# Performance work log

Measured on AMD Instinct MI355X. Metric: run time of the kernel, lower is better.

Reference implementation:

```python
import jax, jax.numpy as jnp
import numpy as np

MARGIN = 0.1


def setup_inputs() -> dict:
    key = jax.random.key(0)
    k1, k2 = jax.random.split(key)
    n, d, n_classes = 8192, 128, 512
    x = jax.random.normal(k1, (n, d), dtype=jnp.float32)
    # L2-normalize embeddings (cosine similarity regime, consistent with 0.6 threshold)
    x = x / jnp.linalg.norm(x, axis=1, keepdims=True)
    targets = jax.random.randint(k2, (n,), 0, n_classes, dtype=jnp.int64)
    return {"inputs": x, "targets": targets}


def reference(inputs, targets):
    n = inputs.shape[0]
    sim = inputs @ inputs.T                                   # [n, n]
    same = targets[:, None] == targets[None, :]               # label equality
    eye = jnp.eye(n, dtype=bool)
    pos_mask = same & ~eye                                    # positives, diag removed
    neg_mask = ~same                                          # negatives (diag excluded: same label)

    neg_inf = jnp.float32(-jnp.inf)
    max_neg = jnp.max(jnp.where(neg_mask, sim, neg_inf), axis=1)   # neg_pair_[-1]
    max_pos = jnp.max(jnp.where(pos_mask, sim, neg_inf), axis=1)   # pos_pair_[-1]

    # select positives with sim < max_neg + margin ; loss = sum(1 - sim)
    pos_sel = pos_mask & (sim < (max_neg + MARGIN)[:, None])
    pos_loss = jnp.sum(jnp.where(pos_sel, 1.0 - sim, 0.0), axis=1)

    # select negatives with sim > max(0.6, max_pos) - margin ; loss = sum(sim)
    thr = jnp.maximum(jnp.float32(0.6), max_pos) - MARGIN
    neg_sel = neg_mask & (sim > thr[:, None])
    neg_loss = jnp.sum(jnp.where(neg_sel, sim, 0.0), axis=1)

    has_pos = jnp.any(pos_mask, axis=1)
    loss = jnp.sum(jnp.where(has_pos, pos_loss + neg_loss, 0.0)) / n

    # diagnostics from the last row (as in the torch code's trailing pos_pair_/neg_pair_)
    lp = pos_mask[-1]
    ln = neg_mask[-1]
    mean_pos_sim = jnp.sum(jnp.where(lp, sim[-1], 0.0)) / jnp.maximum(jnp.sum(lp), 1)
    mean_neg_sim = jnp.sum(jnp.where(ln, sim[-1], 0.0)) / jnp.maximum(jnp.sum(ln), 1)
    zero = jnp.float32(0.0)
    return (loss, zero, zero, zero, mean_pos_sim, mean_neg_sim)
```

## Files before the change

### kernel.cpp

```cpp
#include <hip/hip_runtime.h>

typedef __attribute__((ext_vector_type(8))) short short8;
typedef __attribute__((ext_vector_type(4))) float f32x4;

#define D 128
#define MARGIN 0.1f
#define MAXC 64
#define FCAP 256

__device__ __forceinline__ unsigned short f32_to_bf16(float f) {
  unsigned int u = __float_as_uint(f);
  u += 0x7fffu + ((u >> 16) & 1u);
  return (unsigned short)(u >> 16);
}
__device__ __forceinline__ unsigned fkey(float f) {
  unsigned b = __float_as_uint(f);
  return b ^ (((unsigned)((int)b >> 31)) | 0x80000000u);
}
__device__ __forceinline__ float fdec(unsigned k) {
  unsigned b = k ^ ((k & 0x80000000u) ? 0x80000000u : 0xFFFFFFFFu);
  return __uint_as_float(b);
}

__global__ void k_prep(const float* __restrict__ x, unsigned short* __restrict__ xb,
                       unsigned* __restrict__ mn_u, int* __restrict__ cls_cnt, int n) {
  int gid = blockIdx.x * 256 + threadIdx.x;
  int i = gid * 4;
  float4 v = *reinterpret_cast<const float4*>(x + i);
  ushort4 o;
  o.x = f32_to_bf16(v.x);
  o.y = f32_to_bf16(v.y);
  o.z = f32_to_bf16(v.z);
  o.w = f32_to_bf16(v.w);
  *reinterpret_cast<ushort4*>(xb + i) = o;
  if (gid < n) mn_u[gid] = 0u;
  if (gid < 512) cls_cnt[gid] = 0;
}

#define MF(A, B, C) __builtin_amdgcn_mfma_f32_16x16x32_bf16(A, B, C, 0, 0, 0)

__launch_bounds__(256)
__global__ void k_main(const unsigned short* __restrict__ xb, const int* __restrict__ tg,
                       unsigned* __restrict__ mn_u,
                       int* __restrict__ cls_cnt, int* __restrict__ cls_idx, int n) {
  const int nrb = n >> 8;
  const int ngemm = nrb * 16;
  const int tid = threadIdx.x;
  if ((int)blockIdx.x >= ngemm) {
    int i = ((int)blockIdx.x - ngemm) * 256 + tid;
    if (i < n) {
      int c = tg[i];
      int s = atomicAdd(&cls_cnt[c], 1);
      if (s < MAXC) cls_idx[c * MAXC + s] = i;
    }
    return;
  }

  __shared__ uint4 ldsbuf[4096];
  char* lds = (char*)ldsbuf;
  const int lane = tid & 63;
  const int wid = tid >> 6;
  const int rb = blockIdx.x % nrb;
  const int colpart = blockIdx.x / nrb;
  const int r0 = rb << 8;
  const int cg = lane & 15;
  const int agrp = lane >> 4;

  short8 a[4][4];
#pragma unroll
  for (int rt = 0; rt < 4; ++rt)
#pragma unroll
    for (int kk = 0; kk < 4; ++kk)
      a[rt][kk] = *reinterpret_cast<const short8*>(
          xb + (size_t)(r0 + wid * 64 + rt * 16 + cg) * D + kk * 32 + agrp * 8);

  float mn[4][4];
#pragma unroll
  for (int rt = 0; rt < 4; ++rt)
#pragma unroll
    for (int reg = 0; reg < 4; ++reg) mn[rt][reg] = -INFINITY;

  const int skey = (((tid >> 4) & 7) << 4);
  const char* gbase = (const char*)xb + (size_t)colpart * 512 * 256;

  {
    uint4 v[8];
#pragma unroll
    for (int q = 0; q < 8; ++q)
      v[q] = *reinterpret_cast<const uint4*>(gbase + q * 4096 + tid * 16);
#pragma unroll
    for (int q = 0; q < 8; ++q)
      *reinterpret_cast<uint4*>(lds + ((q * 4096 + tid * 16) ^ skey)) = v[q];
  }
  __syncthreads();

  const int rowbase = r0 + wid * 64 + agrp * 4;

  int rofs[4];
#pragma unroll
  for (int kk = 0; kk < 4; ++kk)
    rofs[kk] = (cg * 256 + agrp * 16 + kk * 64) ^ ((cg & 7) << 4);

#pragma unroll
  for (int s = 0; s < 4; ++s) {
    uint4 g[8];
    if (s + 1 < 4) {
      const char* gs = gbase + (size_t)(s + 1) * 32768;
#pragma unroll
      for (int q = 0; q < 8; ++q)
        g[q] = *reinterpret_cast<const uint4*>(gs + q * 4096 + tid * 16);
    }
    const char* bb = lds + (s & 1) * 32768;
    const int cs = colpart * 4 + s;
    const bool hasdiag = ((cs >> 1) == rb);
    if (!hasdiag) {
#pragma unroll
      for (int j = 0; j < 8; ++j) {
        const char* tb = bb + j * 4096;
        short8 B[4];
#pragma unroll
        for (int kk = 0; kk < 4; ++kk)
          B[kk] = *reinterpret_cast<const short8*>(tb + rofs[kk]);
#pragma unroll
        for (int rt = 0; rt < 4; ++rt) {
          f32x4 acc = {0.f, 0.f, 0.f, 0.f};
          acc = MF(a[rt][0], B[0], acc);
          acc = MF(a[rt][1], B[1], acc);
          acc = MF(a[rt][2], B[2], acc);
          acc = MF(a[rt][3], B[3], acc);
#pragma unroll
          for (int reg = 0; reg < 4; ++reg)
            mn[rt][reg] = fmaxf(mn[rt][reg], acc[reg]);
        }
      }
    } else {
      const int ebase = rowbase - ((cs << 7) + cg);
#pragma unroll
      for (int j = 0; j < 8; ++j) {
        const char* tb = bb + j * 4096;
        short8 B[4];
#pragma unroll
        for (int kk = 0; kk < 4; ++kk)
          B[kk] = *reinterpret_cast<const short8*>(tb + rofs[kk]);
        const int e = ebase - j * 16;
#pragma unroll
        for (int rt = 0; rt < 4; ++rt) {
          f32x4 acc = {0.f, 0.f, 0.f, 0.f};
          acc = MF(a[rt][0], B[0], acc);
          acc = MF(a[rt][1], B[1], acc);
          acc = MF(a[rt][2], B[2], acc);
          acc = MF(a[rt][3], B[3], acc);
#pragma unroll
          for (int reg = 0; reg < 4; ++reg) {
            float v = (e + rt * 16 + reg == 0) ? -INFINITY : acc[reg];
            mn[rt][reg] = fmaxf(mn[rt][reg], v);
          }
        }
      }
    }
    if (s + 1 < 4) {
      char* wb = lds + ((s + 1) & 1) * 32768;
#pragma unroll
      for (int q = 0; q < 8; ++q)
        *reinterpret_cast<uint4*>(wb + ((q * 4096 + tid * 16) ^ skey)) = g[q];
      __syncthreads();
    }
  }

#pragma unroll
  for (int m = 1; m < 16; m <<= 1)
#pragma unroll
    for (int rt = 0; rt < 4; ++rt)
#pragma unroll
      for (int reg = 0; reg < 4; ++reg)
        mn[rt][reg] = fmaxf(mn[rt][reg], __shfl_xor(mn[rt][reg], m, 16));

  if (cg == 0) {
#pragma unroll
    for (int rt = 0; rt < 4; ++rt)
#pragma unroll
      for (int reg = 0; reg < 4; ++reg)
        atomicMax(&mn_u[rowbase + rt * 16 + reg], fkey(mn[rt][reg]));
  }
}

__global__ void k_posdiag(const float* __restrict__ x, const int* __restrict__ tg,
                          const unsigned* __restrict__ mn_u,
                          const int* __restrict__ cls_cnt, const int* __restrict__ cls_idx,
                          float* __restrict__ thn, float* __restrict__ pos_part,
                          float* __restrict__ dpart, int n) {
  __shared__ float red2[4][4];
  int lane = threadIdx.x & 63, wid = threadIdx.x >> 6;
  int nposb = n / 4;
  if ((int)blockIdx.x < nposb) {
    int r = blockIdx.x * 4 + wid;
    int tr = tg[r];
    float2 xr = *reinterpret_cast<const float2*>(x + (size_t)r * D + lane * 2);
    float thp = fdec(mn_u[r]) + MARGIN;
    int cnt = cls_cnt[tr];
    int m = cnt < MAXC ? cnt : MAXC;
    float mpos = -INFINITY, pl = 0.f;
    for (int k = 0; k < m; ++k) {
      int j = cls_idx[tr * MAXC + k];
      if (j == r) continue;
      float2 xj = *reinterpret_cast<const float2*>(x + (size_t)j * D + lane * 2);
      float d = xr.x * xj.x + xr.y * xj.y;
#pragma unroll
      for (int mm = 1; mm < 64; mm <<= 1) d += __shfl_xor(d, mm, 64);
      mpos = fmaxf(mpos, d);
      if (d < thp) pl += 1.0f - d;
    }
    bool has_pos = cnt > 1;
    if (lane == 0) {
      thn[r] = has_pos ? (fmaxf(0.6f, mpos) - MARGIN) : INFINITY;
      pos_part[r] = has_pos ? pl : 0.f;
    }
  } else {
    int col = (blockIdx.x - nposb) * 256 + threadIdx.x;
    int R = n - 1;
    int tR = tg[R];
    const float4* xr = reinterpret_cast<const float4*>(x + (size_t)R * D);
    const float4* xc = reinterpret_cast<const float4*>(x + (size_t)col * D);
    float dot = 0.f;
#pragma unroll
    for (int k = 0; k < D / 4; ++k) {
      float4 va = xr[k], vb = xc[k];
      dot += va.x * vb.x + va.y * vb.y + va.z * vb.z + va.w * vb.w;
    }
    int t = tg[col];
    bool same = (t == tR);
    bool isR = (col == R);
    float v[4];
    v[0] = (same && !isR) ? dot : 0.f;
    v[1] = (same && !isR) ? 1.f : 0.f;
    v[2] = (!same) ? dot : 0.f;
    v[3] = (!same) ? 1.f : 0.f;
#pragma unroll
    for (int m = 1; m < 64; m <<= 1)
#pragma unroll
      for (int j = 0; j < 4; ++j) v[j] += __shfl_xor(v[j], m, 64);
    if (lane == 0) {
#pragma unroll
      for (int j = 0; j < 4; ++j) red2[wid][j] = v[j];
    }
    __syncthreads();
    if (threadIdx.x == 0) {
#pragma unroll
      for (int j = 0; j < 4; ++j)
        dpart[(blockIdx.x - nposb) * 4 + j] =
            red2[0][j] + red2[1][j] + red2[2][j] + red2[3][j];
    }
  }
}

__global__ void k_final(const float* __restrict__ x, const int* __restrict__ tg,
                        const float* __restrict__ pos_part,
                        const unsigned* __restrict__ mn_u, const float* __restrict__ thn,
                        const float* __restrict__ dpart, int ndiag,
                        float* __restrict__ out, int n) {
  __shared__ int flags[FCAP];
  __shared__ int nflag;
  if (threadIdx.x == 0) nflag = 0;
  __syncthreads();
  float s = 0.f;
  for (int i = threadIdx.x; i < n; i += 256) {
    s += pos_part[i];
    if (fdec(mn_u[i]) > thn[i] - 0.02f) {
      int k = atomicAdd(&nflag, 1);
      if (k < FCAP) flags[k] = i;
    }
  }
  __syncthreads();
  int m = nflag < FCAP ? nflag : FCAP;
  for (int f = 0; f < m; ++f) {
    int r = flags[f];
    int trr = tg[r];
    float tv = thn[r];
    const float4* xr = reinterpret_cast<const float4*>(x + (size_t)r * D);
    for (int c = threadIdx.x; c < n; c += 256) {
      if (tg[c] == trr) continue;
      const float4* xc = reinterpret_cast<const float4*>(x + (size_t)c * D);
      float dot = 0.f;
#pragma unroll
      for (int k = 0; k < D / 4; ++k) {
        float4 va = xr[k], vb = xc[k];
        dot += va.x * vb.x + va.y * vb.y + va.z * vb.z + va.w * vb.w;
      }
      if (dot > tv) s += dot;
    }
  }
  int lane = threadIdx.x & 63, wid = threadIdx.x >> 6;
#pragma unroll
  for (int mm = 1; mm < 64; mm <<= 1) s += __shfl_xor(s, mm, 64);
  __shared__ float red[4];
  if (lane == 0) red[wid] = s;
  __syncthreads();
  if (threadIdx.x == 0) {
    float loss = red[0] + red[1] + red[2] + red[3];
    float ps = 0.f, pc = 0.f, ns = 0.f, nc = 0.f;
    for (int b = 0; b < ndiag; ++b) {
      ps += dpart[b * 4 + 0];
      pc += dpart[b * 4 + 1];
      ns += dpart[b * 4 + 2];
      nc += dpart[b * 4 + 3];
    }
    out[0] = loss / (float)n;
    out[1] = 0.f;
    out[2] = 0.f;
    out[3] = 0.f;
    out[4] = ps / fmaxf(pc, 1.f);
    out[5] = ns / fmaxf(nc, 1.f);
  }
}

extern "C" void kernel_launch(void* const* d_in, const int* in_sizes, int n_in,
                              void* d_out, int out_size, void* d_ws, size_t ws_size,
                              hipStream_t stream) {
  const float* x = (const float*)d_in[0];
  const int* tg = (const int*)d_in[1];
  float* out = (float*)d_out;
  int n = in_sizes[1];

  char* ws = (char*)d_ws;
  unsigned short* xb = (unsigned short*)ws;
  size_t off = (size_t)n * D * 2;
  unsigned* mn_u = (unsigned*)(ws + off); off += (size_t)n * 4;
  float* thn = (float*)(ws + off); off += (size_t)n * 4;
  int* cls_cnt = (int*)(ws + off); off += 512 * 4;
  int* cls_idx = (int*)(ws + off); off += 512 * MAXC * 4;
  float* pos_part = (float*)(ws + off); off += (size_t)n * 4;
  float* dpart = (float*)(ws + off);

  int total = n * D;
  int nrb = n >> 8;
  int ngemm = nrb * 16;
  k_prep<<<total / 1024, 256, 0, stream>>>(x, xb, mn_u, cls_cnt, n);
  k_main<<<ngemm + nrb, 256, 0, stream>>>(xb, tg, mn_u, cls_cnt, cls_idx, n);
  int nposb = n / 4, ndiag = n / 256;
  k_posdiag<<<nposb + ndiag, 256, 0, stream>>>(x, tg, mn_u, cls_cnt, cls_idx,
                                               thn, pos_part, dpart, n);
  k_final<<<1, 256, 0, stream>>>(x, tg, pos_part, mn_u, thn, dpart, ndiag, out, n);
}
```

Before: 72.72 us.

## Fuse all stages into one cooperative persistent kernel with grid syncs

Replaces the four separate kernel launches (prep, GEMM-max, positive/diagonal, final) with a single cooperative kernel of 256 blocks that separates the stages with grid-wide syncs. Each block now covers twice as many column stripes in the GEMM stage and two rounds of rows in the positive stage, which uses 16-lane groups instead of full waves. This removes launch gaps and inter-kernel overhead. In exchange, grid.sync costs are added, the GEMM runs with only 256 blocks at lower occupancy, and the sizes are hardcoded for n=8192.

```diff
diff --git a/kernel.cpp b/kernel.cpp
--- a/kernel.cpp
+++ b/kernel.cpp
@@ -1,4 +1,7 @@
 #include <hip/hip_runtime.h>
+#include <hip/hip_cooperative_groups.h>
+
+namespace cg = cooperative_groups;
 
 typedef __attribute__((ext_vector_type(8))) short short8;
 typedef __attribute__((ext_vector_type(4))) float f32x4;
@@ -22,294 +25,297 @@
   return __uint_as_float(b);
 }
 
-__global__ void k_prep(const float* __restrict__ x, unsigned short* __restrict__ xb,
-                       unsigned* __restrict__ mn_u, int* __restrict__ cls_cnt, int n) {
-  int gid = blockIdx.x * 256 + threadIdx.x;
-  int i = gid * 4;
-  float4 v = *reinterpret_cast<const float4*>(x + i);
-  ushort4 o;
-  o.x = f32_to_bf16(v.x);
-  o.y = f32_to_bf16(v.y);
-  o.z = f32_to_bf16(v.z);
-  o.w = f32_to_bf16(v.w);
-  *reinterpret_cast<ushort4*>(xb + i) = o;
-  if (gid < n) mn_u[gid] = 0u;
-  if (gid < 512) cls_cnt[gid] = 0;
-}
-
 #define MF(A, B, C) __builtin_amdgcn_mfma_f32_16x16x32_bf16(A, B, C, 0, 0, 0)
 
 __launch_bounds__(256)
-__global__ void k_main(const unsigned short* __restrict__ xb, const int* __restrict__ tg,
-                       unsigned* __restrict__ mn_u,
-                       int* __restrict__ cls_cnt, int* __restrict__ cls_idx, int n) {
-  const int nrb = n >> 8;
-  const int ngemm = nrb * 16;
+__global__ void k_all(const float* __restrict__ x, const int* __restrict__ tg,
+                      unsigned short* __restrict__ xb, unsigned* __restrict__ mn_u,
+                      float* __restrict__ thn, int* __restrict__ cls_cnt,
+                      int* __restrict__ cls_idx, float* __restrict__ pos_part,
+                      float* __restrict__ dpart, float* __restrict__ out, int n) {
+  cg::grid_group grid = cg::this_grid();
+  __shared__ uint4 ldsbuf[4096];
+  __shared__ float red2[4][4];
+  __shared__ float redf[4];
+  __shared__ int flags[FCAP];
+  __shared__ int nflag;
+
   const int tid = threadIdx.x;
-  if ((int)blockIdx.x >= ngemm) {
-    int i = ((int)blockIdx.x - ngemm) * 256 + tid;
-    if (i < n) {
+  const int bid = blockIdx.x;
+  const int gid = bid * 256 + tid;
+  const int lane = tid & 63;
+  const int wid = tid >> 6;
+
+  {
+    int i0 = gid * 16;
+#pragma unroll
+    for (int q = 0; q < 4; ++q) {
+      float4 v = *reinterpret_cast<const float4*>(x + i0 + q * 4);
+      ushort4 o;
+      o.x = f32_to_bf16(v.x);
+      o.y = f32_to_bf16(v.y);
+      o.z = f32_to_bf16(v.z);
+      o.w = f32_to_bf16(v.w);
+      *reinterpret_cast<ushort4*>(xb + i0 + q * 4) = o;
+    }
+    if (gid < n) mn_u[gid] = 0u;
+    if (gid < 512) cls_cnt[gid] = 0;
+  }
+  grid.sync();
+
+  {
+    if (tid < 32) {
+      int i = bid * 32 + tid;
       int c = tg[i];
       int s = atomicAdd(&cls_cnt[c], 1);
       if (s < MAXC) cls_idx[c * MAXC + s] = i;
     }
-    return;
-  }
-
-  __shared__ uint4 ldsbuf[4096];
-  char* lds = (char*)ldsbuf;
-  const int lane = tid & 63;
-  const int wid = tid >> 6;
-  const int rb = blockIdx.x % nrb;
-  const int colpart = blockIdx.x / nrb;
-  const int r0 = rb << 8;
-  const int cg = lane & 15;
-  const int agrp = lane >> 4;
-
-  short8 a[4][4];
-#pragma unroll
-  for (int rt = 0; rt < 4; ++rt)
+
+    const int nrb = n >> 8;
+    const int rb = bid % nrb;
+    const int cp0 = bid / nrb;
+    const int r0 = rb << 8;
+    const int cgl = lane & 15;
+    const int agrp = lane >> 4;
+    char* lds = (char*)ldsbuf;
+
+    short8 a[4][4];
+#pragma unroll
+    for (int rt = 0; rt < 4; ++rt)
+#pragma unroll
+      for (int kk = 0; kk < 4; ++kk)
+        a[rt][kk] = *reinterpret_cast<const short8*>(
+            xb + (size_t)(r0 + wid * 64 + rt * 16 + cgl) * D + kk * 32 + agrp * 8);
+
+    float mn[4][4];
+#pragma unroll
+    for (int rt = 0; rt < 4; ++rt)
+#pragma unroll
+      for (int reg = 0; reg < 4; ++reg) mn[rt][reg] = -INFINITY;
+
+    const int skey = (((tid >> 4) & 7) << 4);
+    const int rowbase = r0 + wid * 64 + agrp * 4;
+
+#define CS_OF(s) ((((s) < 4) ? cp0 : cp0 + 8) * 4 + ((s) & 3))
+
+    {
+      const char* gs = (const char*)xb + (size_t)CS_OF(0) * 32768;
+      uint4 v[8];
+#pragma unroll
+      for (int q = 0; q < 8; ++q)
+        v[q] = *reinterpret_cast<const uint4*>(gs + q * 4096 + tid * 16);
+#pragma unroll
+      for (int q = 0; q < 8; ++q)
+        *reinterpret_cast<uint4*>(lds + ((q * 4096 + tid * 16) ^ skey)) = v[q];
+    }
+    __syncthreads();
+
+    int rofs[4];
 #pragma unroll
     for (int kk = 0; kk < 4; ++kk)
-      a[rt][kk] = *reinterpret_cast<const short8*>(
-          xb + (size_t)(r0 + wid * 64 + rt * 16 + cg) * D + kk * 32 + agrp * 8);
-
-  float mn[4][4];
-#pragma unroll
-  for (int rt = 0; rt < 4; ++rt)
-#pragma unroll
-    for (int reg = 0; reg < 4; ++reg) mn[rt][reg] = -INFINITY;
-
-  const int skey = (((tid >> 4) & 7) << 4);
-  const char* gbase = (const char*)xb + (size_t)colpart * 512 * 256;
-
-  {
-    uint4 v[8];
-#pragma unroll
-    for (int q = 0; q < 8; ++q)
-      v[q] = *reinterpret_cast<const uint4*>(gbase + q * 4096 + tid * 16);
-#pragma unroll
-    for (int q = 0; q < 8; ++q)
-      *reinterpret_cast<uint4*>(lds + ((q * 4096 + tid * 16) ^ skey)) = v[q];
-  }
-  __syncthreads();
-
-  const int rowbase = r0 + wid * 64 + agrp * 4;
-
-  int rofs[4];
-#pragma unroll
-  for (int kk = 0; kk < 4; ++kk)
-    rofs[kk] = (cg * 256 + agrp * 16 + kk * 64) ^ ((cg & 7) << 4);
-
-#pragma unroll
-  for (int s = 0; s < 4; ++s) {
-    uint4 g[8];
-    if (s + 1 < 4) {
-      const char* gs = gbase + (size_t)(s + 1) * 32768;
-#pragma unroll
-      for (int q = 0; q < 8; ++q)
-        g[q] = *reinterpret_cast<const uint4*>(gs + q * 4096 + tid * 16);
-    }
-    const char* bb = lds + (s & 1) * 32768;
-    const int cs = colpart * 4 + s;
-    const bool hasdiag = ((cs >> 1) == rb);
-    if (!hasdiag) {
-#pragma unroll
-      for (int j = 0; j < 8; ++j) {
-        const char* tb = bb + j * 4096;
-        short8 B[4];
-#pragma unroll
-        for (int kk = 0; kk < 4; ++kk)
-          B[kk] = *reinterpret_cast<const short8*>(tb + rofs[kk]);
-#pragma unroll
-        for (int rt = 0; rt < 4; ++rt) {
-          f32x4 acc = {0.f, 0.f, 0.f, 0.f};
-          acc = MF(a[rt][0], B[0], acc);
-          acc = MF(a[rt][1], B[1], acc);
-          acc = MF(a[rt][2], B[2], acc);
-          acc = MF(a[rt][3], B[3], acc);
-#pragma unroll
-          for (int reg = 0; reg < 4; ++reg)
-            mn[rt][reg] = fmaxf(mn[rt][reg], acc[reg]);
-        }
-      }
-    } else {
-      const int ebase = rowbase - ((cs << 7) + cg);
-#pragma unroll
-      for (int j = 0; j < 8; ++j) {
-        const char* tb = bb + j * 4096;
-        short8 B[4];
-#pragma unroll
-        for (int kk = 0; kk < 4; ++kk)
-          B[kk] = *reinterpret_cast<const short8*>(tb + rofs[kk]);
-        const int e = ebase - j * 16;
-#pragma unroll
-        for (int rt = 0; rt < 4; ++rt) {
-          f32x4 acc = {0.f, 0.f, 0.f, 0.f};
-          acc = MF(a[rt][0], B[0], acc);
-          acc = MF(a[rt][1], B[1], acc);
-          acc = MF(a[rt][2], B[2], acc);
-          acc = MF(a[rt][3], B[3], acc);
-#pragma unroll
-          for (int reg = 0; reg < 4; ++reg) {
-            float v = (e + rt * 16 + reg == 0) ? -INFINITY : acc[reg];
-            mn[rt][reg] = fmaxf(mn[rt][reg], v);
+      rofs[kk] = (cgl * 256 + agrp * 16 + kk * 64) ^ ((cgl & 7) << 4);
+
+    for (int s = 0; s < 8; ++s) {
+      uint4 g[8];
+      if (s + 1 < 8) {
+        const char* gs = (const char*)xb + (size_t)CS_OF(s + 1) * 32768;
+#pragma unroll
+        for (int q = 0; q < 8; ++q)
+          g[q] = *reinterpret_cast<const uint4*>(gs + q * 4096 + tid * 16);
+      }
+      const char* bb = lds + (s & 1) * 32768;
+      const int cs = CS_OF(s);
+      const bool hasdiag = ((cs >> 1) == rb);
+      if (!hasdiag) {
+#pragma unroll
+        for (int j = 0; j < 8; ++j) {
+          const char* tb = bb + j * 4096;
+          short8 B[4];
+#pragma unroll
+          for (int kk = 0; kk < 4; ++kk)
+            B[kk] = *reinterpret_cast<const short8*>(tb + rofs[kk]);
+#pragma unroll
+          for (int rt = 0; rt < 4; ++rt) {
+            f32x4 acc = {0.f, 0.f, 0.f, 0.f};
+            acc = MF(a[rt][0], B[0], acc);
+            acc = MF(a[rt][1], B[1], acc);
+            acc = MF(a[rt][2], B[2], acc);
+            acc = MF(a[rt][3], B[3], acc);
+#pragma unroll
+            for (int reg = 0; reg < 4; ++reg)
+              mn[rt][reg] = fmaxf(mn[rt][reg], acc[reg]);
           }
         }
-      }
-    }
-    if (s + 1 < 4) {
-      char* wb = lds + ((s + 1) & 1) * 32768;
-#pragma unroll
-      for (int q = 0; q < 8; ++q)
-        *reinterpret_cast<uint4*>(wb + ((q * 4096 + tid * 16) ^ skey)) = g[q];
-      __syncthreads();
+      } else {
+        const int ebase = rowbase - ((cs << 7) + cgl);
+#pragma unroll
+        for (int j = 0; j < 8; ++j) {
+          const char* tb = bb + j * 4096;
+          short8 B[4];
+#pragma unroll
+          for (int kk = 0; kk < 4; ++kk)
+            B[kk] = *reinterpret_cast<const short8*>(tb + rofs[kk]);
+          const int e = ebase - j * 16;
+#pragma unroll
+          for (int rt = 0; rt < 4; ++rt) {
+            f32x4 acc = {0.f, 0.f, 0.f, 0.f};
+            acc = MF(a[rt][0], B[0], acc);
+            acc = MF(a[rt][1], B[1], acc);
+            acc = MF(a[rt][2], B[2], acc);
+            acc = MF(a[rt][3], B[3], acc);
+#pragma unroll
+            for (int reg = 0; reg < 4; ++reg) {
+              float v = (e + rt * 16 + reg == 0) ? -INFINITY : acc[reg];
+              mn[rt][reg] = fmaxf(mn[rt][reg], v);
+            }
+          }
+        }
+      }
+      if (s + 1 < 8) {
+        char* wb = lds + ((s + 1) & 1) * 32768;
+#pragma unroll
+        for (int q = 0; q < 8; ++q)
+          *reinterpret_cast<uint4*>(wb + ((q * 4096 + tid * 16) ^ skey)) = g[q];
+        __syncthreads();
+      }
+    }
+
+#pragma unroll
+    for (int m = 1; m < 16; m <<= 1)
+#pragma unroll
+      for (int rt = 0; rt < 4; ++rt)
+#pragma unroll
+        for (int reg = 0; reg < 4; ++reg)
+          mn[rt][reg] = fmaxf(mn[rt][reg], __shfl_xor(mn[rt][reg], m, 16));
+
+    if (cgl == 0) {
+#pragma unroll
+      for (int rt = 0; rt < 4; ++rt)
+#pragma unroll
+        for (int reg = 0; reg < 4; ++reg)
+          atomicMax(&mn_u[rowbase + rt * 16 + reg], fkey(mn[rt][reg]));
     }
   }
-
-#pragma unroll
-  for (int m = 1; m < 16; m <<= 1)
-#pragma unroll
-    for (int rt = 0; rt < 4; ++rt)
-#pragma unroll
-      for (int reg = 0; reg < 4; ++reg)
-        mn[rt][reg] = fmaxf(mn[rt][reg], __shfl_xor(mn[rt][reg], m, 16));
-
-  if (cg == 0) {
-#pragma unroll
-    for (int rt = 0; rt < 4; ++rt)
-#pragma unroll
-      for (int reg = 0; reg < 4; ++reg)
-        atomicMax(&mn_u[rowbase + rt * 16 + reg], fkey(mn[rt][reg]));
-  }
-}
-
-__global__ void k_posdiag(const float* __restrict__ x, const int* __restrict__ tg,
-                          const unsigned* __restrict__ mn_u,
-                          const int* __restrict__ cls_cnt, const int* __restrict__ cls_idx,
-                          float* __restrict__ thn, float* __restrict__ pos_part,
-                          float* __restrict__ dpart, int n) {
-  __shared__ float red2[4][4];
-  int lane = threadIdx.x & 63, wid = threadIdx.x >> 6;
-  int nposb = n / 4;
-  if ((int)blockIdx.x < nposb) {
-    int r = blockIdx.x * 4 + wid;
-    int tr = tg[r];
-    float2 xr = *reinterpret_cast<const float2*>(x + (size_t)r * D + lane * 2);
-    float thp = fdec(mn_u[r]) + MARGIN;
-    int cnt = cls_cnt[tr];
-    int m = cnt < MAXC ? cnt : MAXC;
-    float mpos = -INFINITY, pl = 0.f;
-    for (int k = 0; k < m; ++k) {
-      int j = cls_idx[tr * MAXC + k];
-      if (j == r) continue;
-      float2 xj = *reinterpret_cast<const float2*>(x + (size_t)j * D + lane * 2);
-      float d = xr.x * xj.x + xr.y * xj.y;
-#pragma unroll
-      for (int mm = 1; mm < 64; mm <<= 1) d += __shfl_xor(d, mm, 64);
-      mpos = fmaxf(mpos, d);
-      if (d < thp) pl += 1.0f - d;
-    }
-    bool has_pos = cnt > 1;
-    if (lane == 0) {
-      thn[r] = has_pos ? (fmaxf(0.6f, mpos) - MARGIN) : INFINITY;
-      pos_part[r] = has_pos ? pl : 0.f;
-    }
-  } else {
-    int col = (blockIdx.x - nposb) * 256 + threadIdx.x;
-    int R = n - 1;
-    int tR = tg[R];
-    const float4* xr = reinterpret_cast<const float4*>(x + (size_t)R * D);
-    const float4* xc = reinterpret_cast<const float4*>(x + (size_t)col * D);
-    float dot = 0.f;
-#pragma unroll
-    for (int k = 0; k < D / 4; ++k) {
-      float4 va = xr[k], vb = xc[k];
-      dot += va.x * vb.x + va.y * vb.y + va.z * vb.z + va.w * vb.w;
-    }
-    int t = tg[col];
-    bool same = (t == tR);
-    bool isR = (col == R);
-    float v[4];
-    v[0] = (same && !isR) ? dot : 0.f;
-    v[1] = (same && !isR) ? 1.f : 0.f;
-    v[2] = (!same) ? dot : 0.f;
-    v[3] = (!same) ? 1.f : 0.f;
-#pragma unroll
-    for (int m = 1; m < 64; m <<= 1)
-#pragma unroll
-      for (int j = 0; j < 4; ++j) v[j] += __shfl_xor(v[j], m, 64);
-    if (lane == 0) {
-#pragma unroll
-      for (int j = 0; j < 4; ++j) red2[wid][j] = v[j];
-    }
-    __syncthreads();
-    if (threadIdx.x == 0) {
-#pragma unroll
-      for (int j = 0; j < 4; ++j)
-        dpart[(blockIdx.x - nposb) * 4 + j] =
-            red2[0][j] + red2[1][j] + red2[2][j] + red2[3][j];
-    }
-  }
-}
-
-__global__ void k_final(const float* __restrict__ x, const int* __restrict__ tg,
-                        const float* __restrict__ pos_part,
-                        const unsigned* __restrict__ mn_u, const float* __restrict__ thn,
-                        const float* __restrict__ dpart, int ndiag,
-                        float* __restrict__ out, int n) {
-  __shared__ int flags[FCAP];
-  __shared__ int nflag;
-  if (threadIdx.x == 0) nflag = 0;
-  __syncthreads();
-  float s = 0.f;
-  for (int i = threadIdx.x; i < n; i += 256) {
-    s += pos_part[i];
-    if (fdec(mn_u[i]) > thn[i] - 0.02f) {
-      int k = atomicAdd(&nflag, 1);
-      if (k < FCAP) flags[k] = i;
-    }
-  }
-  __syncthreads();
-  int m = nflag < FCAP ? nflag : FCAP;
-  for (int f = 0; f < m; ++f) {
-    int r = flags[f];
-    int trr = tg[r];
-    float tv = thn[r];
-    const float4* xr = reinterpret_cast<const float4*>(x + (size_t)r * D);
-    for (int c = threadIdx.x; c < n; c += 256) {
-      if (tg[c] == trr) continue;
-      const float4* xc = reinterpret_cast<const float4*>(x + (size_t)c * D);
+  grid.sync();
+
+  {
+    const int g16 = lane >> 4;
+    const int l16 = lane & 15;
+    for (int round = 0; round < 2; ++round) {
+      int r = round * 4096 + bid * 16 + wid * 4 + g16;
+      int tr = tg[r];
+      float4 xr0 = *reinterpret_cast<const float4*>(x + (size_t)r * D + l16 * 8);
+      float4 xr1 = *reinterpret_cast<const float4*>(x + (size_t)r * D + l16 * 8 + 4);
+      float thp = fdec(mn_u[r]) + MARGIN;
+      int cnt = cls_cnt[tr];
+      int m = cnt < MAXC ? cnt : MAXC;
+      float mpos = -INFINITY, pl = 0.f;
+      for (int k = 0; k < m; ++k) {
+        int j = cls_idx[tr * MAXC + k];
+        if (j == r) continue;
+        float4 a0 = *reinterpret_cast<const float4*>(x + (size_t)j * D + l16 * 8);
+        float4 a1 = *reinterpret_cast<const float4*>(x + (size_t)j * D + l16 * 8 + 4);
+        float d = xr0.x * a0.x + xr0.y * a0.y + xr0.z * a0.z + xr0.w * a0.w +
+                  xr1.x * a1.x + xr1.y * a1.y + xr1.z * a1.z + xr1.w * a1.w;
+#pragma unroll
+        for (int mm = 1; mm < 16; mm <<= 1) d += __shfl_xor(d, mm, 16);
+        mpos = fmaxf(mpos, d);
+        if (d < thp) pl += 1.0f - d;
+      }
+      bool has_pos = cnt > 1;
+      if (l16 == 0) {
+        thn[r] = has_pos ? (fmaxf(0.6f, mpos) - MARGIN) : INFINITY;
+        pos_part[r] = has_pos ? pl : 0.f;
+      }
+    }
+    if (bid < (n >> 8)) {
+      int col = bid * 256 + tid;
+      int R = n - 1;
+      int tR = tg[R];
+      const float4* xr = reinterpret_cast<const float4*>(x + (size_t)R * D);
+      const float4* xc = reinterpret_cast<const float4*>(x + (size_t)col * D);
       float dot = 0.f;
 #pragma unroll
       for (int k = 0; k < D / 4; ++k) {
         float4 va = xr[k], vb = xc[k];
         dot += va.x * vb.x + va.y * vb.y + va.z * vb.z + va.w * vb.w;
       }
-      if (dot > tv) s += dot;
+      int t = tg[col];
+      bool same = (t == tR);
+      bool isR = (col == R);
+      float v[4];
+      v[0] = (same && !isR) ? dot : 0.f;
+      v[1] = (same && !isR) ? 1.f : 0.f;
+      v[2] = (!same) ? dot : 0.f;
+      v[3] = (!same) ? 1.f : 0.f;
+#pragma unroll
+      for (int m = 1; m < 64; m <<= 1)
+#pragma unroll
+        for (int j = 0; j < 4; ++j) v[j] += __shfl_xor(v[j], m, 64);
+      if (lane == 0) {
+#pragma unroll
+        for (int j = 0; j < 4; ++j) red2[wid][j] = v[j];
+      }
+      __syncthreads();
+      if (tid == 0) {
+#pragma unroll
+        for (int j = 0; j < 4; ++j)
+          dpart[bid * 4 + j] = red2[0][j] + red2[1][j] + red2[2][j] + red2[3][j];
+      }
     }
   }
-  int lane = threadIdx.x & 63, wid = threadIdx.x >> 6;
-#pragma unroll
-  for (int mm = 1; mm < 64; mm <<= 1) s += __shfl_xor(s, mm, 64);
-  __shared__ float red[4];
-  if (lane == 0) red[wid] = s;
-  __syncthreads();
-  if (threadIdx.x == 0) {
-    float loss = red[0] + red[1] + red[2] + red[3];
-    float ps = 0.f, pc = 0.f, ns = 0.f, nc = 0.f;
-    for (int b = 0; b < ndiag; ++b) {
-      ps += dpart[b * 4 + 0];
-      pc += dpart[b * 4 + 1];
-      ns += dpart[b * 4 + 2];
-      nc += dpart[b * 4 + 3];
-    }
-    out[0] = loss / (float)n;
-    out[1] = 0.f;
-    out[2] = 0.f;
-    out[3] = 0.f;
-    out[4] = ps / fmaxf(pc, 1.f);
-    out[5] = ns / fmaxf(nc, 1.f);
+  grid.sync();
+
+  if (bid == 0) {
+    if (tid == 0) nflag = 0;
+    __syncthreads();
+    float s = 0.f;
+    for (int i = tid; i < n; i += 256) {
+      s += pos_part[i];
+      if (fdec(mn_u[i]) > thn[i] - 0.02f) {
+        int k = atomicAdd(&nflag, 1);
+        if (k < FCAP) flags[k] = i;
+      }
+    }
+    __syncthreads();
+    int m = nflag < FCAP ? nflag : FCAP;
+    for (int f = 0; f < m; ++f) {
+      int r = flags[f];
+      int trr = tg[r];
+      float tv = thn[r];
+      const float4* xr = reinterpret_cast<const float4*>(x + (size_t)r * D);
+      for (int c = tid; c < n; c += 256) {
+        if (tg[c] == trr) continue;
+        const float4* xc = reinterpret_cast<const float4*>(x + (size_t)c * D);
+        float dot = 0.f;
+#pragma unroll
+        for (int k = 0; k < D / 4; ++k) {
+          float4 va = xr[k], vb = xc[k];
+          dot += va.x * vb.x + va.y * vb.y + va.z * vb.z + va.w * vb.w;
+        }
+        if (dot > tv) s += dot;
+      }
+    }
+#pragma unroll
+    for (int mm = 1; mm < 64; mm <<= 1) s += __shfl_xor(s, mm, 64);
+    if (lane == 0) redf[wid] = s;
+    __syncthreads();
+    if (tid == 0) {
+      float loss = redf[0] + redf[1] + redf[2] + redf[3];
+      float ps = 0.f, pc = 0.f, ns = 0.f, nc = 0.f;
+      for (int b = 0; b < (n >> 8); ++b) {
+        ps += dpart[b * 4 + 0];
+        pc += dpart[b * 4 + 1];
+        ns += dpart[b * 4 + 2];
+        nc += dpart[b * 4 + 3];
+      }
+      out[0] = loss / (float)n;
+      out[1] = 0.f;
+      out[2] = 0.f;
+      out[3] = 0.f;
+      out[4] = ps / fmaxf(pc, 1.f);
+      out[5] = ns / fmaxf(nc, 1.f);
+    }
   }
 }
 
@@ -331,13 +337,8 @@
   float* pos_part = (float*)(ws + off); off += (size_t)n * 4;
   float* dpart = (float*)(ws + off);
 
-  int total = n * D;
-  int nrb = n >> 8;
-  int ngemm = nrb * 16;
-  k_prep<<<total / 1024, 256, 0, stream>>>(x, xb, mn_u, cls_cnt, n);
-  k_main<<<ngemm + nrb, 256, 0, stream>>>(xb, tg, mn_u, cls_cnt, cls_idx, n);
-  int nposb = n / 4, ndiag = n / 256;
-  k_posdiag<<<nposb + ndiag, 256, 0, stream>>>(x, tg, mn_u, cls_cnt, cls_idx,
-                                               thn, pos_part, dpart, n);
-  k_final<<<1, 256, 0, stream>>>(x, tg, pos_part, mn_u, thn, dpart, ndiag, out, n);
-}
+  void* args[] = {(void*)&x, (void*)&tg, (void*)&xb, (void*)&mn_u, (void*)&thn,
+                  (void*)&cls_cnt, (void*)&cls_idx, (void*)&pos_part,
+                  (void*)&dpart, (void*)&out, (void*)&n};
+  hipLaunchCooperativeKernel((void*)k_all, dim3(256), dim3(256), args, 0, stream);
+}
```

New measurement: 180.5 us. +148.2%, slower.

## Use 512-thread GEMM blocks, fold class bucketing in, fuse final reduction via last-block

Applied to the files above, without the earlier changes.

The max-negative GEMM kernel now uses 512-thread blocks covering 512 rows each, so every LDS-staged column tile is reused by twice as many rows and fewer blocks are launched. Class bucketing is moved into the first row-block GEMM blocks instead of separate trailing blocks. The single-block final kernel is removed and its work now runs in whichever pos/diag block finishes last, detected with a global atomic counter and fences, saving one launch. The trade-offs are fewer blocks for the GEMM (possibly lower occupancy or imbalance) and the serial tail work now sitting inside the larger kernel.

```diff
diff --git a/kernel.cpp b/kernel.cpp
--- a/kernel.cpp
+++ b/kernel.cpp
@@ -23,7 +23,8 @@
 }
 
 __global__ void k_prep(const float* __restrict__ x, unsigned short* __restrict__ xb,
-                       unsigned* __restrict__ mn_u, int* __restrict__ cls_cnt, int n) {
+                       unsigned* __restrict__ mn_u, int* __restrict__ cls_cnt,
+                       int* __restrict__ done_cnt, int n) {
   int gid = blockIdx.x * 256 + threadIdx.x;
   int i = gid * 4;
   float4 v = *reinterpret_cast<const float4*>(x + i);
@@ -35,36 +36,33 @@
   *reinterpret_cast<ushort4*>(xb + i) = o;
   if (gid < n) mn_u[gid] = 0u;
   if (gid < 512) cls_cnt[gid] = 0;
+  if (gid == 0) done_cnt[0] = 0;
 }
 
 #define MF(A, B, C) __builtin_amdgcn_mfma_f32_16x16x32_bf16(A, B, C, 0, 0, 0)
 
-__launch_bounds__(256)
+__launch_bounds__(512)
 __global__ void k_main(const unsigned short* __restrict__ xb, const int* __restrict__ tg,
                        unsigned* __restrict__ mn_u,
                        int* __restrict__ cls_cnt, int* __restrict__ cls_idx, int n) {
-  const int nrb = n >> 8;
-  const int ngemm = nrb * 16;
-  const int tid = threadIdx.x;
-  if ((int)blockIdx.x >= ngemm) {
-    int i = ((int)blockIdx.x - ngemm) * 256 + tid;
-    if (i < n) {
-      int c = tg[i];
-      int s = atomicAdd(&cls_cnt[c], 1);
-      if (s < MAXC) cls_idx[c * MAXC + s] = i;
-    }
-    return;
-  }
-
   __shared__ uint4 ldsbuf[4096];
   char* lds = (char*)ldsbuf;
+  const int tid = threadIdx.x;
+  const int nrb = n >> 9;
+  const int rb = blockIdx.x % nrb;
+  const int cp = blockIdx.x / nrb;
   const int lane = tid & 63;
   const int wid = tid >> 6;
-  const int rb = blockIdx.x % nrb;
-  const int colpart = blockIdx.x / nrb;
-  const int r0 = rb << 8;
-  const int cg = lane & 15;
+  const int r0 = rb << 9;
+  const int cgl = lane & 15;
   const int agrp = lane >> 4;
+
+  if ((int)blockIdx.x < nrb) {
+    int i = blockIdx.x * 512 + tid;
+    int c = tg[i];
+    int s = atomicAdd(&cls_cnt[c], 1);
+    if (s < MAXC) cls_idx[c * MAXC + s] = i;
+  }
 
   short8 a[4][4];
 #pragma unroll
@@ -72,7 +70,7 @@
 #pragma unroll
     for (int kk = 0; kk < 4; ++kk)
       a[rt][kk] = *reinterpret_cast<const short8*>(
-          xb + (size_t)(r0 + wid * 64 + rt * 16 + cg) * D + kk * 32 + agrp * 8);
+          xb + (size_t)(r0 + wid * 64 + rt * 16 + cgl) * D + kk * 32 + agrp * 8);
 
   float mn[4][4];
 #pragma unroll
@@ -81,16 +79,16 @@
     for (int reg = 0; reg < 4; ++reg) mn[rt][reg] = -INFINITY;
 
   const int skey = (((tid >> 4) & 7) << 4);
-  const char* gbase = (const char*)xb + (size_t)colpart * 512 * 256;
+  const char* gbase = (const char*)xb + (size_t)cp * 512 * 256;
 
   {
-    uint4 v[8];
-#pragma unroll
-    for (int q = 0; q < 8; ++q)
-      v[q] = *reinterpret_cast<const uint4*>(gbase + q * 4096 + tid * 16);
-#pragma unroll
-    for (int q = 0; q < 8; ++q)
-      *reinterpret_cast<uint4*>(lds + ((q * 4096 + tid * 16) ^ skey)) = v[q];
+    uint4 v[4];
+#pragma unroll
+    for (int q = 0; q < 4; ++q)
+      v[q] = *reinterpret_cast<const uint4*>(gbase + q * 8192 + tid * 16);
+#pragma unroll
+    for (int q = 0; q < 4; ++q)
+      *reinterpret_cast<uint4*>(lds + ((q * 8192 + tid * 16) ^ skey)) = v[q];
   }
   __syncthreads();
 
@@ -99,20 +97,20 @@
   int rofs[4];
 #pragma unroll
   for (int kk = 0; kk < 4; ++kk)
-    rofs[kk] = (cg * 256 + agrp * 16 + kk * 64) ^ ((cg & 7) << 4);
+    rofs[kk] = (cgl * 256 + agrp * 16 + kk * 64) ^ ((cgl & 7) << 4);
 
 #pragma unroll
   for (int s = 0; s < 4; ++s) {
-    uint4 g[8];
+    uint4 g[4];
     if (s + 1 < 4) {
       const char* gs = gbase + (size_t)(s + 1) * 32768;
 #pragma unroll
-      for (int q = 0; q < 8; ++q)
-        g[q] = *reinterpret_cast<const uint4*>(gs + q * 4096 + tid * 16);
+      for (int q = 0; q < 4; ++q)
+        g[q] = *reinterpret_cast<const uint4*>(gs + q * 8192 + tid * 16);
     }
     const char* bb = lds + (s & 1) * 32768;
-    const int cs = colpart * 4 + s;
-    const bool hasdiag = ((cs >> 1) == rb);
+    const int cs = cp * 4 + s;
+    const bool hasdiag = ((cs >> 2) == rb);
     if (!hasdiag) {
 #pragma unroll
       for (int j = 0; j < 8; ++j) {
@@ -134,7 +132,7 @@
         }
       }
     } else {
-      const int ebase = rowbase - ((cs << 7) + cg);
+      const int ebase = rowbase - ((cs << 7) + cgl);
 #pragma unroll
       for (int j = 0; j < 8; ++j) {
         const char* tb = bb + j * 4096;
@@ -161,8 +159,8 @@
     if (s + 1 < 4) {
       char* wb = lds + ((s + 1) & 1) * 32768;
 #pragma unroll
-      for (int q = 0; q < 8; ++q)
-        *reinterpret_cast<uint4*>(wb + ((q * 4096 + tid * 16) ^ skey)) = g[q];
+      for (int q = 0; q < 4; ++q)
+        *reinterpret_cast<uint4*>(wb + ((q * 8192 + tid * 16) ^ skey)) = g[q];
       __syncthreads();
     }
   }
@@ -175,7 +173,7 @@
       for (int reg = 0; reg < 4; ++reg)
         mn[rt][reg] = fmaxf(mn[rt][reg], __shfl_xor(mn[rt][reg], m, 16));
 
-  if (cg == 0) {
+  if (cgl == 0) {
 #pragma unroll
     for (int rt = 0; rt < 4; ++rt)
 #pragma unroll
@@ -188,10 +186,15 @@
                           const unsigned* __restrict__ mn_u,
                           const int* __restrict__ cls_cnt, const int* __restrict__ cls_idx,
                           float* __restrict__ thn, float* __restrict__ pos_part,
-                          float* __restrict__ dpart, int n) {
+                          float* __restrict__ dpart, int* __restrict__ done_cnt,
+                          float* __restrict__ out, int n) {
   __shared__ float red2[4][4];
+  __shared__ int flags[FCAP];
+  __shared__ int nflag;
+  __shared__ int myrank;
   int lane = threadIdx.x & 63, wid = threadIdx.x >> 6;
-  int nposb = n / 4;
+  int nposb = n / 4, ndiag = n / 256;
+  int nblocks = nposb + ndiag;
   if ((int)blockIdx.x < nposb) {
     int r = blockIdx.x * 4 + wid;
     int tr = tg[r];
@@ -251,15 +254,14 @@
             red2[0][j] + red2[1][j] + red2[2][j] + red2[3][j];
     }
   }
-}
-
-__global__ void k_final(const float* __restrict__ x, const int* __restrict__ tg,
-                        const float* __restrict__ pos_part,
-                        const unsigned* __restrict__ mn_u, const float* __restrict__ thn,
-                        const float* __restrict__ dpart, int ndiag,
-                        float* __restrict__ out, int n) {
-  __shared__ int flags[FCAP];
-  __shared__ int nflag;
+
+  __syncthreads();
+  __threadfence();
+  if (threadIdx.x == 0) myrank = atomicAdd(done_cnt, 1);
+  __syncthreads();
+  if (myrank != nblocks - 1) return;
+  __threadfence();
+
   if (threadIdx.x == 0) nflag = 0;
   __syncthreads();
   float s = 0.f;
@@ -289,14 +291,13 @@
       if (dot > tv) s += dot;
     }
   }
-  int lane = threadIdx.x & 63, wid = threadIdx.x >> 6;
 #pragma unroll
   for (int mm = 1; mm < 64; mm <<= 1) s += __shfl_xor(s, mm, 64);
-  __shared__ float red[4];
-  if (lane == 0) red[wid] = s;
+  __shared__ float redf[4];
+  if (lane == 0) redf[wid] = s;
   __syncthreads();
   if (threadIdx.x == 0) {
-    float loss = red[0] + red[1] + red[2] + red[3];
+    float loss = redf[0] + redf[1] + redf[2] + redf[3];
     float ps = 0.f, pc = 0.f, ns = 0.f, nc = 0.f;
     for (int b = 0; b < ndiag; ++b) {
       ps += dpart[b * 4 + 0];
@@ -329,15 +330,14 @@
   int* cls_cnt = (int*)(ws + off); off += 512 * 4;
   int* cls_idx = (int*)(ws + off); off += 512 * MAXC * 4;
   float* pos_part = (float*)(ws + off); off += (size_t)n * 4;
+  int* done_cnt = (int*)(ws + off); off += 64;
   float* dpart = (float*)(ws + off);
 
   int total = n * D;
-  int nrb = n >> 8;
-  int ngemm = nrb * 16;
-  k_prep<<<total / 1024, 256, 0, stream>>>(x, xb, mn_u, cls_cnt, n);
-  k_main<<<ngemm + nrb, 256, 0, stream>>>(xb, tg, mn_u, cls_cnt, cls_idx, n);
+  int nrb = n >> 9;
+  k_prep<<<total / 1024, 256, 0, stream>>>(x, xb, mn_u, cls_cnt, done_cnt, n);
+  k_main<<<nrb * 16, 512, 0, stream>>>(xb, tg, mn_u, cls_cnt, cls_idx, n);
   int nposb = n / 4, ndiag = n / 256;
   k_posdiag<<<nposb + ndiag, 256, 0, stream>>>(x, tg, mn_u, cls_cnt, cls_idx,
-                                               thn, pos_part, dpart, n);
-  k_final<<<1, 256, 0, stream>>>(x, tg, pos_part, mn_u, thn, dpart, ndiag, out, n);
-}
+                                               thn, pos_part, dpart, done_cnt, out, n);
+}
```

Result: slower. 209.0 us (+187.4%).
